# Optimization experiments

Hardware: AMD Instinct MI355X
Metric: run time of the kernel (lower is better)

Reference implementation:

```python
import jax, jax.numpy as jnp
import numpy as np

B, N, E, D, M, T, P, HS, HN, C, NH = 64, 1024, 512, 1024, 16, 12, 2048, 2048, 64, 4, 8
EPS = 1e-8


def _ln(x, g, b):
    m = x.mean(-1, keepdims=True)
    v = ((x - m) ** 2).mean(-1, keepdims=True)
    return (x - m) / jnp.sqrt(v + 1e-5) * g + b


def _glu(x):
    a, b = jnp.split(x, 2, axis=-1)
    return a * jax.nn.sigmoid(b)


def setup_inputs() -> dict:
    key = jax.random.key(0)
    ks = jax.random.split(key, 24)
    s = 0.02
    rn = lambda k, sh: jax.random.normal(k, sh, jnp.float32) * s
    inp = {
        'kv_tokens': jax.random.normal(ks[0], (B, N, E), jnp.float32),
        'raw_r_act': jnp.full((P,), -10.0, jnp.float32),  # no_decay_init
        'raw_r_out': jnp.full((P,), -10.0, jnp.float32),
        'q_w': rn(ks[1], (E, P)), 'q_b': jnp.zeros((E,), jnp.float32),
        'in_proj_w': rn(ks[2], (3 * E, E)), 'in_proj_b': jnp.zeros((3 * E,), jnp.float32),
        'out_proj_w': rn(ks[3], (E, E)), 'out_proj_b': jnp.zeros((E,), jnp.float32),
        'z_ln_g': jnp.ones((D,), jnp.float32), 'z_ln_b': jnp.zeros((D,), jnp.float32),
        'o_ln_g': jnp.ones((E,), jnp.float32), 'o_ln_b': jnp.zeros((E,), jnp.float32),
        'gate_w': rn(ks[4], (D, D + E)), 'gate_b': jnp.zeros((D,), jnp.float32),
        'cand_w': rn(ks[5], (D, D + E)), 'cand_b': jnp.zeros((D,), jnp.float32),
        'syn1_w': rn(ks[6], (HS, D + E)), 'syn1_b': jnp.zeros((HS,), jnp.float32),
        'syn2_w': rn(ks[7], (D, HS)), 'syn2_b': jnp.zeros((D,), jnp.float32),
        'nlm1_w': rn(ks[8], (D, M, 2 * HN)), 'nlm1_b': jnp.zeros((D, 2 * HN), jnp.float32),
        'nlm2_w': rn(ks[9], (D, HN, 2)), 'nlm2_b': jnp.zeros((D, 2), jnp.float32),
        'head_w': rn(ks[10], (C, P)), 'head_b': jnp.zeros((C,), jnp.float32),
        'act_left': jax.random.randint(ks[11], (P,), 0, D),
        'act_right': jax.random.randint(ks[12], (P,), 0, D),
        'out_left': jax.random.randint(ks[13], (P,), 0, D),
        'out_right': jax.random.randint(ks[14], (P,), 0, D),
    }
    return inp


def reference(kv_tokens, raw_r_act, raw_r_out, q_w, q_b, in_proj_w, in_proj_b,
              out_proj_w, out_proj_b, z_ln_g, z_ln_b, o_ln_g, o_ln_b,
              gate_w, gate_b, cand_w, cand_b, syn1_w, syn1_b, syn2_w, syn2_b,
              nlm1_w, nlm1_b, nlm2_w, nlm2_b, head_w, head_b,
              act_left, act_right, out_left, out_right):
    dh = E // NH
    scale = 1.0 / np.sqrt(dh).astype(np.float32)
    Wq, Wk, Wv = jnp.split(in_proj_w, 3, axis=0)
    bq, bk, bv = jnp.split(in_proj_b, 3, axis=0)
    # K/V are tick-invariant: project once.
    k = (kv_tokens @ Wk.T + bk).reshape(B, N, NH, dh).transpose(0, 2, 1, 3)  # [B,H,N,dh]
    v = (kv_tokens @ Wv.T + bv).reshape(B, N, NH, dh).transpose(0, 2, 1, 3)
    decay_a = jnp.exp(-jax.nn.softplus(raw_r_act))[None, :]
    decay_o = jnp.exp(-jax.nn.softplus(raw_r_out))[None, :]

    z0 = jnp.zeros((B, D), kv_tokens.dtype)
    A0 = jnp.zeros((B, D, M), kv_tokens.dtype)
    # init_state with z0 == 0 -> alpha 0, beta 1, synch 0
    a_a0 = z0[:, act_left] * z0[:, act_right]
    b_a0 = jnp.ones_like(a_a0)
    s_a0 = a_a0 / jnp.sqrt(b_a0 + EPS)
    a_o0 = z0[:, out_left] * z0[:, out_right]
    b_o0 = jnp.ones_like(a_o0)

    def tick(carry, _):
        z, A, a_a, b_a, s_a, a_o, b_o = carry
        # attention query from action sync
        q = s_a @ q_w.T + q_b                                  # [B,E]
        qh = (q @ Wq.T + bq).reshape(B, NH, 1, dh)
        scores = jnp.einsum('bhqd,bhnd->bhqn', qh, k) * scale  # [B,H,1,N]
        attn = jax.nn.softmax(scores, axis=-1)
        o = jnp.einsum('bhqn,bhnd->bhqd', attn, v).reshape(B, E)
        o = o @ out_proj_w.T + out_proj_b
        o = _ln(o, o_ln_g, o_ln_b)                             # LN on o
        zn = _ln(z, z_ln_g, z_ln_b)                            # LN on z
        # gated fusion
        u = jnp.concatenate([zn, o], axis=-1)
        g = jax.nn.sigmoid(u @ gate_w.T + gate_b)
        h = jnp.tanh(u @ cand_w.T + cand_b)
        z_bar = (1.0 - g) * zn + g * h
        fused = jnp.concatenate([z_bar, o], axis=-1)           # [B,D+E]
        # synapse MLP -> pre-activation
        pre = jax.nn.gelu(fused @ syn1_w.T + syn1_b, approximate=False) @ syn2_w.T + syn2_b
        A = jnp.concatenate([A[:, :, 1:], pre[:, :, None]], axis=-1)  # shift history
        # deep NLM (per-neuron SuperLinear + GLU, twice)
        h1 = _glu(jnp.einsum('bdm,dmh->bdh', A, nlm1_w) + nlm1_b)
        z = _glu(jnp.einsum('bdh,dho->bdo', h1, nlm2_w) + nlm2_b)[..., 0]
        # decayed pair synchronisation updates
        a_a = decay_a * a_a + z[:, act_left] * z[:, act_right]
        b_a = decay_a * b_a + 1.0
        s_a = a_a / jnp.sqrt(b_a + EPS)
        a_o = decay_o * a_o + z[:, out_left] * z[:, out_right]
        b_o = decay_o * b_o + 1.0
        s_o = a_o / jnp.sqrt(b_o + EPS)
        logits = s_o @ head_w.T + head_b                       # [B,C]
        return (z, A, a_a, b_a, s_a, a_o, b_o), (logits, z)

    carry0 = (z0, A0, a_a0, b_a0, s_a0, a_o0, b_o0)
    _, (logits_t, z_t) = jax.lax.scan(tick, carry0, None, length=T)
    logits_ticks = jnp.transpose(logits_t, (1, 2, 0))          # [B,C,T]
    p = jnp.clip(jax.nn.softmax(logits_ticks, axis=1), 1e-8, None)
    ent = -(p * jnp.log(p)).sum(axis=1)
    certainty = 1.0 - ent / np.float32(np.log(C))              # [B,T]
    z_ticks = jnp.transpose(z_t, (1, 0, 2))                    # [B,T,D]
    return logits_ticks, certainty, z_ticks
```

## Files before the change

### kernel.cpp

```cpp
#include <hip/hip_runtime.h>
#include <hip/hip_bf16.h>

#define B_ 64
#define N_ 1024
#define E_ 512
#define D_ 1024
#define M_ 16
#define T_ 12
#define P_ 2048
#define HS_ 2048
#define HN_ 64
#define C_ 4
#define NH_ 8
#define DH_ 64

typedef __attribute__((ext_vector_type(8))) short bf16x8;
typedef __attribute__((ext_vector_type(4))) float f32x4;

__device__ __forceinline__ float bf2f(unsigned int u) {
    union { unsigned int i; float f; } c; c.i = (u & 0xffffu) << 16; return c.f;
}
__device__ __forceinline__ unsigned short f2bf(float f) {
    union { float f; unsigned int i; } c; c.f = f;
    unsigned int x = c.i;
    unsigned int r = x + 0x7fffu + ((x >> 16) & 1u);
    return (unsigned short)(r >> 16);
}

__global__ void init_kernel(unsigned short* s_a_bf, float* a_a, float* b_a, float* a_o, float* b_o, float* z) {
    int i = blockIdx.x * 256 + threadIdx.x;
    if (i < B_ * P_) { a_a[i] = 0.f; b_a[i] = 1.f; a_o[i] = 0.f; b_o[i] = 1.f; s_a_bf[i] = 0; }
    if (i < B_ * D_) z[i] = 0.f;
}

__global__ __launch_bounds__(256) void cvt_bf16_kernel(const float* __restrict__ in,
                                                       unsigned short* __restrict__ out, int n4) {
    int i = blockIdx.x * 256 + threadIdx.x;
    if (i < n4) {
        float4 v = ((const float4*)in)[i];
        ushort4 o;
        o.x = f2bf(v.x); o.y = f2bf(v.y); o.z = f2bf(v.z); o.w = f2bf(v.w);
        ((ushort4*)out)[i] = o;
    }
}

__global__ __launch_bounds__(256) void cvt_ilv_kernel(const float* __restrict__ g,
                                                      const float* __restrict__ c,
                                                      unsigned short* __restrict__ out) {
    int r = blockIdx.x;
    const float* src = (r & 1) ? (c + (size_t)(r >> 1) * 1536) : (g + (size_t)(r >> 1) * 1536);
    for (int k = threadIdx.x * 4; k < 1536; k += 1024) {
        float4 v = *(const float4*)(src + k);
        ushort4 o;
        o.x = f2bf(v.x); o.y = f2bf(v.y); o.z = f2bf(v.z); o.w = f2bf(v.w);
        *(ushort4*)(out + (size_t)r * 1536 + k) = o;
    }
}

__global__ __launch_bounds__(256) void transpose_cvt_kernel(const float* __restrict__ in,
                                                            unsigned short* __restrict__ out,
                                                            int R, int Ccols) {
    __shared__ float tb[32][33];
    int c0 = blockIdx.x * 32, r0 = blockIdx.y * 32;
    int tx = threadIdx.x & 31, ty = threadIdx.x >> 5;
#pragma unroll
    for (int i = 0; i < 32; i += 8) tb[ty + i][tx] = in[(size_t)(r0 + ty + i) * Ccols + c0 + tx];
    __syncthreads();
#pragma unroll
    for (int i = 0; i < 32; i += 8) out[(size_t)(c0 + ty + i) * R + r0 + tx] = f2bf(tb[tx][ty + i]);
}

__global__ __launch_bounds__(256) void bcomb_kernel(const float* __restrict__ in_proj_w,
                                                    const float* __restrict__ in_proj_b,
                                                    const float* __restrict__ q_b,
                                                    float* __restrict__ bc) {
    int e = blockIdx.x * 256 + threadIdx.x;
    if (e < E_) {
        const float* wr = in_proj_w + (size_t)e * E_;
        float s = in_proj_b[e];
        for (int k = 0; k < E_; k += 4) {
            float4 w4 = *(const float4*)(wr + k);
            float4 q4 = *(const float4*)(q_b + k);
            s += w4.x * q4.x + w4.y * q4.y + w4.z * q4.z + w4.w * q4.w;
        }
        bc[e] = s;
    }
}

template <bool HAS_BIAS>
__global__ __launch_bounds__(256) void gemm_bt_kernel(const unsigned short* __restrict__ A,
                                                      const unsigned short* __restrict__ Bt,
                                                      const float* __restrict__ bias,
                                                      unsigned short* __restrict__ C,
                                                      int M, int N, int K) {
    __shared__ __align__(16) unsigned short ldsA[2][4096];
    __shared__ __align__(16) unsigned short ldsB[2][4096];
    int id = blockIdx.y * gridDim.x + blockIdx.x;
    int nwg = gridDim.x * gridDim.y;
    int swz = (id & 7) * (nwg >> 3) + (id >> 3);
    int bx = swz % gridDim.x, by = swz / gridDim.x;
    int m0 = by * 128;
    int n0 = bx * 128;
    int tid = threadIdx.x;
    int wv = tid >> 6, l = tid & 63;
    int wr = wv >> 1, wc = wv & 1;
    int lr = l & 15, lg = l >> 4;
    f32x4 acc[4][4] = {};

    auto stage = [&](int buf, int kt) {
        int k0 = kt * 32;
#pragma unroll
        for (int i = 0; i < 2; i++) {
            int tsk = tid + 256 * i;
            int r = tsk >> 2, g = tsk & 3;
            int gs = (g ^ (r & 3)) * 8;
            __builtin_amdgcn_global_load_lds(
                (const __attribute__((address_space(1))) void*)(A + (size_t)(m0 + r) * K + k0 + gs),
                (__attribute__((address_space(3))) void*)&ldsA[buf][tsk * 8], 16, 0, 0);
        }
#pragma unroll
        for (int i = 0; i < 2; i++) {
            int tsk = tid + 256 * i;
            int r = tsk >> 2, g = tsk & 3;
            int gs = (g ^ (r & 3)) * 8;
            __builtin_amdgcn_global_load_lds(
                (const __attribute__((address_space(1))) void*)(Bt + (size_t)(n0 + r) * K + k0 + gs),
                (__attribute__((address_space(3))) void*)&ldsB[buf][tsk * 8], 16, 0, 0);
        }
    };

    int nt = K >> 5;
    stage(0, 0);
    for (int t = 0; t < nt; t++) {
        int cur = t & 1;
        if (t + 1 < nt) {
            stage(cur ^ 1, t + 1);
            asm volatile("s_waitcnt vmcnt(4)" ::: "memory");
        } else {
            asm volatile("s_waitcnt vmcnt(0)" ::: "memory");
        }
        __builtin_amdgcn_s_barrier();
        bf16x8 af[4], bfr[4];
#pragma unroll
        for (int mi = 0; mi < 4; mi++) {
            int r = wr * 64 + mi * 16 + lr;
            af[mi] = *(const bf16x8*)&ldsA[cur][r * 32 + ((lg ^ (r & 3)) << 3)];
        }
#pragma unroll
        for (int ni = 0; ni < 4; ni++) {
            int c = wc * 64 + ni * 16 + lr;
            bfr[ni] = *(const bf16x8*)&ldsB[cur][c * 32 + ((lg ^ (c & 3)) << 3)];
        }
#pragma unroll
        for (int mi = 0; mi < 4; mi++)
#pragma unroll
            for (int ni = 0; ni < 4; ni++)
                acc[mi][ni] = __builtin_amdgcn_mfma_f32_16x16x32_bf16(af[mi], bfr[ni], acc[mi][ni], 0, 0, 0);
        __builtin_amdgcn_s_barrier();
    }
#pragma unroll
    for (int ni = 0; ni < 4; ni++) {
        int col = n0 + wc * 64 + ni * 16 + lr;
        float bv = HAS_BIAS ? bias[col] : 0.0f;
#pragma unroll
        for (int mi = 0; mi < 4; mi++) {
            int row = m0 + wr * 64 + mi * 16 + lg * 4;
#pragma unroll
            for (int r = 0; r < 4; r++) {
                C[(size_t)(row + r) * N + col] = f2bf(acc[mi][ni][r] + bv);
            }
        }
    }
}

template <int EPI>
__global__ __launch_bounds__(256) void gemmNK_kernel(const unsigned short* __restrict__ A,
                                                     const unsigned short* __restrict__ W,
                                                     const float* __restrict__ bias0,
                                                     const float* __restrict__ bias1,
                                                     const float* __restrict__ zn32,
                                                     void* __restrict__ outp,
                                                     int N, int K) {
    __shared__ __align__(16) unsigned short ldsA[4][2][2048];
    __shared__ __align__(16) unsigned short ldsB[4][2][512];
    int n0 = blockIdx.x * 16;
    int tid = threadIdx.x;
    int w = tid >> 6, l = tid & 63;
    int Kw = K >> 2;
    int kb = w * Kw;
    int lr = l & 15, lg = l >> 4;
    int ar = l >> 2, ag = l & 3;
    f32x4 acc[4] = {};

    auto stage = [&](int buf, int kt) {
        int k0 = kb + (kt << 5);
#pragma unroll
        for (int i = 0; i < 4; i++) {
            int row = i * 16 + ar;
            int gs = (ag ^ (row & 3)) << 3;
            __builtin_amdgcn_global_load_lds(
                (const __attribute__((address_space(1))) void*)(A + (size_t)row * K + k0 + gs),
                (__attribute__((address_space(3))) void*)&ldsA[w][buf][i * 512 + l * 8], 16, 0, 0);
        }
        {
            int col = ar;
            int gs = (ag ^ (col & 3)) << 3;
            __builtin_amdgcn_global_load_lds(
                (const __attribute__((address_space(1))) void*)(W + (size_t)(n0 + col) * K + k0 + gs),
                (__attribute__((address_space(3))) void*)&ldsB[w][buf][l * 8], 16, 0, 0);
        }
    };

    int nt = Kw >> 5;
    stage(0, 0);
    for (int t = 0; t < nt; t++) {
        int cur = t & 1;
        if (t + 1 < nt) {
            stage(cur ^ 1, t + 1);
            asm volatile("s_waitcnt vmcnt(5)" ::: "memory");
        } else {
            asm volatile("s_waitcnt vmcnt(0)" ::: "memory");
        }
        bf16x8 bf = *(const bf16x8*)&ldsB[w][cur][lr * 32 + ((lg ^ (lr & 3)) << 3)];
#pragma unroll
        for (int mi = 0; mi < 4; mi++) {
            int rr = mi * 16 + lr;
            bf16x8 af = *(const bf16x8*)&ldsA[w][cur][rr * 32 + ((lg ^ (rr & 3)) << 3)];
            acc[mi] = __builtin_amdgcn_mfma_f32_16x16x32_bf16(af, bf, acc[mi], 0, 0, 0);
        }
    }
    __syncthreads();
    float* red = (float*)&ldsA[0][0][0];
#pragma unroll
    for (int mi = 0; mi < 4; mi++) {
        int row = mi * 16 + lg * 4;
#pragma unroll
        for (int q = 0; q < 4; q++) red[w * 1024 + (row + q) * 16 + lr] = acc[mi][q];
    }
    __syncthreads();
    int b = tid >> 2, c4 = (tid & 3) << 2;
    f32x4 s = *(f32x4*)&red[b * 16 + c4];
#pragma unroll
    for (int ww = 1; ww < 4; ww++) {
        f32x4 v = *(f32x4*)&red[ww * 1024 + b * 16 + c4];
        s[0] += v[0]; s[1] += v[1]; s[2] += v[2]; s[3] += v[3];
    }
    int col = n0 + c4;
    if (EPI == 0) {
        unsigned short* out = (unsigned short*)outp;
        ushort4 o;
        o.x = f2bf(s[0] + bias0[col + 0]);
        o.y = f2bf(s[1] + bias0[col + 1]);
        o.z = f2bf(s[2] + bias0[col + 2]);
        o.w = f2bf(s[3] + bias0[col + 3]);
        *(ushort4*)(out + (size_t)b * N + col) = o;
    } else if (EPI == 1) {
        float* out = (float*)outp;
        *(f32x4*)(out + (size_t)b * N + col) = s;
    } else if (EPI == 2) {
        unsigned short* out = (unsigned short*)outp;
        int j0 = col >> 1;
#pragma unroll
        for (int pp = 0; pp < 2; pp++) {
            int j = j0 + pp;
            float g = 1.0f / (1.0f + expf(-(s[pp * 2] + bias0[j])));
            float h = tanhf(s[pp * 2 + 1] + bias1[j]);
            float zb = (1.0f - g) * zn32[(size_t)b * D_ + j] + g * h;
            out[(size_t)b * 1536 + j] = f2bf(zb);
        }
    } else if (EPI == 3) {
        unsigned short* out = (unsigned short*)outp;
        ushort4 o;
#pragma unroll
        for (int j = 0; j < 4; j++) {
            float pre = s[j] + bias0[col + j];
            float val = 0.5f * pre * (1.0f + erff(pre * 0.70710678118654752f));
            ((unsigned short*)&o)[j] = f2bf(val);
        }
        *(ushort4*)(out + (size_t)b * N + col) = o;
    } else {
        float* out = (float*)outp;
#pragma unroll
        for (int j = 0; j < 4; j++) {
            out[(size_t)(col + j) * 64 + b] = s[j] + bias0[col + j];
        }
    }
}

__device__ __forceinline__ float wave_max64(float v) {
#pragma unroll
    for (int off = 32; off >= 1; off >>= 1) v = fmaxf(v, __shfl_xor(v, off, 64));
    return v;
}
__device__ __forceinline__ float wave_sum64(float v) {
#pragma unroll
    for (int off = 32; off >= 1; off >>= 1) v += __shfl_xor(v, off, 64);
    return v;
}

__global__ __launch_bounds__(256) void attn_kernel(const unsigned short* __restrict__ kvbuf,
                                                   const unsigned short* __restrict__ qh_bf,
                                                   unsigned short* __restrict__ o_bf) {
    int bh = blockIdx.x;
    int b = bh >> 3, h = bh & 7;
    __shared__ float sc[N_];
    __shared__ float qv[DH_];
    __shared__ float red[8];
    __shared__ float opart[4][DH_];
    int tid = threadIdx.x;
    int w = tid >> 6, lane = tid & 63;
    if (tid < DH_) qv[tid] = bf2f(qh_bf[(size_t)b * E_ + h * DH_ + tid]);
    __syncthreads();
    const unsigned short* kb = kvbuf + (size_t)b * N_ * 1024 + h * DH_;
    float myv[4];
#pragma unroll
    for (int i = 0; i < 4; i++) {
        int n = tid + i * 256;
        const unsigned short* kr = kb + (size_t)n * 1024;
        float s = 0.f;
#pragma unroll
        for (int d = 0; d < DH_; d += 8) {
            uint4 pk = *(const uint4*)(kr + d);
            s += bf2f(pk.x) * qv[d + 0] + bf2f(pk.x >> 16) * qv[d + 1]
               + bf2f(pk.y) * qv[d + 2] + bf2f(pk.y >> 16) * qv[d + 3]
               + bf2f(pk.z) * qv[d + 4] + bf2f(pk.z >> 16) * qv[d + 5]
               + bf2f(pk.w) * qv[d + 6] + bf2f(pk.w >> 16) * qv[d + 7];
        }
        myv[i] = s * 0.125f;
    }
    float m = fmaxf(fmaxf(myv[0], myv[1]), fmaxf(myv[2], myv[3]));
    m = wave_max64(m);
    if (lane == 0) red[w] = m;
    __syncthreads();
    m = fmaxf(fmaxf(red[0], red[1]), fmaxf(red[2], red[3]));
    float s = 0.f;
#pragma unroll
    for (int i = 0; i < 4; i++) {
        float e = expf(myv[i] - m);
        sc[tid + i * 256] = e;
        s += e;
    }
    s = wave_sum64(s);
    if (lane == 0) red[4 + w] = s;
    __syncthreads();
    float inv = 1.0f / (red[4] + red[5] + red[6] + red[7]);
    const unsigned short* vb = kvbuf + (size_t)b * N_ * 1024 + E_ + h * DH_;
    int ng = lane >> 4, d4 = (lane & 15) << 2;
    float a0 = 0.f, a1 = 0.f, a2 = 0.f, a3 = 0.f;
    int n0 = w * 256;
    for (int i = 0; i < 64; i++) {
        int n = n0 + i * 4 + ng;
        uint2 pv = *(const uint2*)(vb + (size_t)n * 1024 + d4);
        float sv = sc[n];
        a0 += sv * bf2f(pv.x);
        a1 += sv * bf2f(pv.x >> 16);
        a2 += sv * bf2f(pv.y);
        a3 += sv * bf2f(pv.y >> 16);
    }
    a0 += __shfl_xor(a0, 16, 64); a0 += __shfl_xor(a0, 32, 64);
    a1 += __shfl_xor(a1, 16, 64); a1 += __shfl_xor(a1, 32, 64);
    a2 += __shfl_xor(a2, 16, 64); a2 += __shfl_xor(a2, 32, 64);
    a3 += __shfl_xor(a3, 16, 64); a3 += __shfl_xor(a3, 32, 64);
    if (lane < 16) {
        opart[w][d4 + 0] = a0;
        opart[w][d4 + 1] = a1;
        opart[w][d4 + 2] = a2;
        opart[w][d4 + 3] = a3;
    }
    __syncthreads();
    if (tid < DH_) {
        float r = (opart[0][tid] + opart[1][tid] + opart[2][tid] + opart[3][tid]) * inv;
        o_bf[(size_t)b * E_ + h * DH_ + tid] = f2bf(r);
    }
}

__global__ __launch_bounds__(256) void reduce_oln_kernel(const float* __restrict__ opre,
                                                         const float* __restrict__ bout,
                                                         const float* __restrict__ og,
                                                         const float* __restrict__ obv,
                                                         const float* __restrict__ z,
                                                         const float* __restrict__ zg,
                                                         const float* __restrict__ zbv,
                                                         unsigned short* __restrict__ u_bf,
                                                         unsigned short* __restrict__ fused_bf,
                                                         float* __restrict__ zn32) {
    int b = blockIdx.x, tid = threadIdx.x;
    __shared__ float red[16];
    float v[2];
#pragma unroll
    for (int i = 0; i < 2; i++) {
        int e = tid + i * 256;
        v[i] = opre[(size_t)b * E_ + e] + bout[e];
    }
    int w = tid >> 6, lane = tid & 63;
    float s1 = v[0] + v[1];
    float s2 = v[0] * v[0] + v[1] * v[1];
#pragma unroll
    for (int off = 32; off >= 1; off >>= 1) { s1 += __shfl_xor(s1, off, 64); s2 += __shfl_xor(s2, off, 64); }
    if (lane == 0) { red[w] = s1; red[4 + w] = s2; }
    __syncthreads();
    s1 = red[0] + red[1] + red[2] + red[3];
    s2 = red[4] + red[5] + red[6] + red[7];
    float mean = s1 * (1.0f / 512.0f);
    float var = s2 * (1.0f / 512.0f) - mean * mean;
    float rstd = 1.0f / sqrtf(var + 1e-5f);
#pragma unroll
    for (int i = 0; i < 2; i++) {
        int e = tid + i * 256;
        unsigned short val = f2bf((v[i] - mean) * rstd * og[e] + obv[e]);
        u_bf[(size_t)b * 1536 + D_ + e] = val;
        fused_bf[(size_t)b * 1536 + D_ + e] = val;
    }
    float zl[4];
    float t1 = 0.f, t2 = 0.f;
#pragma unroll
    for (int i = 0; i < 4; i++) {
        int d = tid + i * 256;
        zl[i] = z[(size_t)b * D_ + d];
        t1 += zl[i]; t2 += zl[i] * zl[i];
    }
#pragma unroll
    for (int off = 32; off >= 1; off >>= 1) { t1 += __shfl_xor(t1, off, 64); t2 += __shfl_xor(t2, off, 64); }
    __syncthreads();
    if (lane == 0) { red[8 + w] = t1; red[12 + w] = t2; }
    __syncthreads();
    t1 = red[8] + red[9] + red[10] + red[11];
    t2 = red[12] + red[13] + red[14] + red[15];
    float zmean = t1 * (1.0f / 1024.0f);
    float zvar = t2 * (1.0f / 1024.0f) - zmean * zmean;
    float zr = 1.0f / sqrtf(zvar + 1e-5f);
#pragma unroll
    for (int i = 0; i < 4; i++) {
        int d = tid + i * 256;
        float zn = (zl[i] - zmean) * zr * zg[d] + zbv[d];
        u_bf[(size_t)b * 1536 + d] = f2bf(zn);
        zn32[(size_t)b * D_ + d] = zn;
    }
}

template <int NT>
__global__ __launch_bounds__(256) void nlm_kernel(const float* __restrict__ AbufT,
                                                  const float* __restrict__ w1g,
                                                  const float* __restrict__ b1g,
                                                  const float* __restrict__ w2g,
                                                  const float* __restrict__ b2g,
                                                  float* __restrict__ z,
                                                  float* __restrict__ zt) {
    __shared__ float w1s[4][2048];
    __shared__ float b1s[4][128];
    __shared__ float w2s[4][128];
    __shared__ float b2s[4][2];
    int tid = threadIdx.x;
    int w = tid >> 6, lane = tid & 63;
    int d = blockIdx.x * 4 + w;
    for (int i = lane; i < 2048; i += 64) w1s[w][i] = w1g[(size_t)d * 2048 + i];
    for (int i = lane; i < 128; i += 64) {
        b1s[w][i] = b1g[(size_t)d * 128 + i];
        w2s[w][i] = w2g[(size_t)d * 128 + i];
    }
    if (lane < 2) b2s[w][lane] = b2g[d * 2 + lane];
    __syncthreads();
    const int b = lane;
    float av[NT];
#pragma unroll
    for (int s = 0; s < NT; s++) av[s] = AbufT[((size_t)s * D_ + d) * 64 + b];
    constexpr int moff = M_ - NT;
    float o0 = b2s[w][0], o1 = b2s[w][1];
    for (int hh = 0; hh < 64; hh++) {
        float a = b1s[w][hh], bb = b1s[w][hh + 64];
#pragma unroll
        for (int s = 0; s < NT; s++) {
            float x = av[s];
            a += x * w1s[w][(s + moff) * 128 + hh];
            bb += x * w1s[w][(s + moff) * 128 + hh + 64];
        }
        float z1 = a / (1.0f + expf(-bb));
        o0 += z1 * w2s[w][hh * 2];
        o1 += z1 * w2s[w][hh * 2 + 1];
    }
    float zv = o0 / (1.0f + expf(-o1));
    z[(size_t)b * D_ + d] = zv;
    zt[((size_t)b * T_ + (NT - 1)) * D_ + d] = zv;
}

__global__ __launch_bounds__(256) void synchead_kernel(const float* __restrict__ z,
                                                       const int* __restrict__ act_l, const int* __restrict__ act_r,
                                                       const int* __restrict__ out_l, const int* __restrict__ out_r,
                                                       const float* __restrict__ raw_a, const float* __restrict__ raw_o,
                                                       const float* __restrict__ head_w, const float* __restrict__ head_b,
                                                       float* __restrict__ a_a, float* __restrict__ b_a,
                                                       unsigned short* __restrict__ s_a_bf,
                                                       float* __restrict__ a_o, float* __restrict__ b_o,
                                                       float* __restrict__ out_logits, float* __restrict__ out_cert, int t) {
    int b = blockIdx.x, tid = threadIdx.x;
    __shared__ float zv[D_];
    __shared__ float red[4][4];
    for (int i = tid; i < D_; i += 256) zv[i] = z[(size_t)b * D_ + i];
    __syncthreads();
    float l0 = 0.f, l1 = 0.f, l2 = 0.f, l3 = 0.f;
    for (int p = tid; p < P_; p += 256) {
        size_t ip = (size_t)b * P_ + p;
        float zl = zv[act_l[p]], zr = zv[act_r[p]];
        float da = 1.0f / (1.0f + expf(raw_a[p]));
        float aa = da * a_a[ip] + zl * zr;
        float ba = da * b_a[ip] + 1.0f;
        a_a[ip] = aa; b_a[ip] = ba;
        s_a_bf[(size_t)b * P_ + p] = f2bf(aa / sqrtf(ba + 1e-8f));
        float zlo = zv[out_l[p]], zro = zv[out_r[p]];
        float dz = 1.0f / (1.0f + expf(raw_o[p]));
        float ao = dz * a_o[ip] + zlo * zro;
        float bo = dz * b_o[ip] + 1.0f;
        a_o[ip] = ao; b_o[ip] = bo;
        float so = ao / sqrtf(bo + 1e-8f);
        l0 += so * head_w[p];
        l1 += so * head_w[P_ + p];
        l2 += so * head_w[2 * P_ + p];
        l3 += so * head_w[3 * P_ + p];
    }
    int w = tid >> 6, lane = tid & 63;
#pragma unroll
    for (int off = 32; off >= 1; off >>= 1) {
        l0 += __shfl_xor(l0, off, 64);
        l1 += __shfl_xor(l1, off, 64);
        l2 += __shfl_xor(l2, off, 64);
        l3 += __shfl_xor(l3, off, 64);
    }
    if (lane == 0) { red[w][0] = l0; red[w][1] = l1; red[w][2] = l2; red[w][3] = l3; }
    __syncthreads();
    if (tid == 0) {
        float lg[4];
#pragma unroll
        for (int c = 0; c < 4; c++) {
            lg[c] = red[0][c] + red[1][c] + red[2][c] + red[3][c] + head_b[c];
            out_logits[((size_t)b * C_ + c) * T_ + t] = lg[c];
        }
        float m = fmaxf(fmaxf(lg[0], lg[1]), fmaxf(lg[2], lg[3]));
        float e0 = expf(lg[0] - m), e1 = expf(lg[1] - m), e2 = expf(lg[2] - m), e3 = expf(lg[3] - m);
        float inv = 1.0f / (e0 + e1 + e2 + e3);
        float ent = 0.f, pp;
        pp = fmaxf(e0 * inv, 1e-8f); ent -= pp * logf(pp);
        pp = fmaxf(e1 * inv, 1e-8f); ent -= pp * logf(pp);
        pp = fmaxf(e2 * inv, 1e-8f); ent -= pp * logf(pp);
        pp = fmaxf(e3 * inv, 1e-8f); ent -= pp * logf(pp);
        out_cert[(size_t)b * T_ + t] = 1.0f - ent * (1.0f / 1.3862943611198906f);
    }
}

extern "C" void kernel_launch(void* const* d_in, const int* in_sizes, int n_in,
                              void* d_out, int out_size, void* d_ws, size_t ws_size,
                              hipStream_t stream) {
    const float* kv_tokens  = (const float*)d_in[0];
    const float* raw_r_act  = (const float*)d_in[1];
    const float* raw_r_out  = (const float*)d_in[2];
    const float* q_w        = (const float*)d_in[3];
    const float* q_b        = (const float*)d_in[4];
    const float* in_proj_w  = (const float*)d_in[5];
    const float* in_proj_b  = (const float*)d_in[6];
    const float* out_proj_w = (const float*)d_in[7];
    const float* out_proj_b = (const float*)d_in[8];
    const float* z_ln_g     = (const float*)d_in[9];
    const float* z_ln_b     = (const float*)d_in[10];
    const float* o_ln_g     = (const float*)d_in[11];
    const float* o_ln_b     = (const float*)d_in[12];
    const float* gate_w     = (const float*)d_in[13];
    const float* gate_b     = (const float*)d_in[14];
    const float* cand_w     = (const float*)d_in[15];
    const float* cand_b     = (const float*)d_in[16];
    const float* syn1_w     = (const float*)d_in[17];
    const float* syn1_b     = (const float*)d_in[18];
    const float* syn2_w     = (const float*)d_in[19];
    const float* syn2_b     = (const float*)d_in[20];
    const float* nlm1_w     = (const float*)d_in[21];
    const float* nlm1_b     = (const float*)d_in[22];
    const float* nlm2_w     = (const float*)d_in[23];
    const float* nlm2_b     = (const float*)d_in[24];
    const float* head_w     = (const float*)d_in[25];
    const float* head_b     = (const float*)d_in[26];
    const int* act_l        = (const int*)d_in[27];
    const int* act_r        = (const int*)d_in[28];
    const int* out_l        = (const int*)d_in[29];
    const int* out_r        = (const int*)d_in[30];

    float* out = (float*)d_out;
    float* out_logits = out;
    float* out_cert = out + B_ * C_ * T_;
    float* out_zt = out_cert + B_ * T_;

    char* ws = (char*)d_ws;
    size_t off = 0;
    auto alloc = [&](size_t bytes) { void* p = ws + off; off += (bytes + 255) & ~(size_t)255; return p; };
    unsigned short* kvbuf   = (unsigned short*)alloc((size_t)B_ * N_ * 1024 * 2);
    unsigned short* kv_bf   = (unsigned short*)alloc((size_t)B_ * N_ * E_ * 2);
    unsigned short* Wkv_bf  = (unsigned short*)alloc((size_t)1024 * E_ * 2);
    unsigned short* Wq_bf   = (unsigned short*)alloc((size_t)E_ * E_ * 2);
    unsigned short* qwT_bf  = (unsigned short*)alloc((size_t)P_ * E_ * 2);
    unsigned short* Wc_bf   = (unsigned short*)alloc((size_t)E_ * P_ * 2);
    unsigned short* Wgc_bf  = (unsigned short*)alloc((size_t)2048 * 1536 * 2);
    unsigned short* Ws1_bf  = (unsigned short*)alloc((size_t)2048 * 1536 * 2);
    unsigned short* Ws2_bf  = (unsigned short*)alloc((size_t)1024 * 2048 * 2);
    unsigned short* Wout_bf = (unsigned short*)alloc((size_t)E_ * E_ * 2);
    float* b_comb = (float*)alloc(E_ * 4);
    unsigned short* s_a_bf  = (unsigned short*)alloc((size_t)B_ * P_ * 2);
    unsigned short* qh_bf   = (unsigned short*)alloc((size_t)B_ * E_ * 2);
    unsigned short* o_bf    = (unsigned short*)alloc((size_t)B_ * E_ * 2);
    unsigned short* u_bf    = (unsigned short*)alloc((size_t)B_ * 1536 * 2);
    unsigned short* fused_bf= (unsigned short*)alloc((size_t)B_ * 1536 * 2);
    unsigned short* tbuf_bf = (unsigned short*)alloc((size_t)B_ * HS_ * 2);
    float* opre = (float*)alloc((size_t)B_ * E_ * 4);
    float* zn32 = (float*)alloc((size_t)B_ * D_ * 4);
    float* a_a  = (float*)alloc((size_t)B_ * P_ * 4);
    float* b_a  = (float*)alloc((size_t)B_ * P_ * 4);
    float* a_o  = (float*)alloc((size_t)B_ * P_ * 4);
    float* b_o  = (float*)alloc((size_t)B_ * P_ * 4);
    float* zbuf = (float*)alloc((size_t)B_ * D_ * 4);
    float* AbufT = (float*)alloc((size_t)T_ * D_ * B_ * 4);

    init_kernel<<<512, 256, 0, stream>>>(s_a_bf, a_a, b_a, a_o, b_o, zbuf);

    cvt_bf16_kernel<<<(1024 * E_ / 4 + 255) / 256, 256, 0, stream>>>(in_proj_w + (size_t)E_ * E_, Wkv_bf, 1024 * E_ / 4);
    cvt_bf16_kernel<<<(E_ * E_ / 4 + 255) / 256, 256, 0, stream>>>(in_proj_w, Wq_bf, E_ * E_ / 4);
    cvt_ilv_kernel<<<2048, 256, 0, stream>>>(gate_w, cand_w, Wgc_bf);
    cvt_bf16_kernel<<<(2048 * 1536 / 4 + 255) / 256, 256, 0, stream>>>(syn1_w, Ws1_bf, 2048 * 1536 / 4);
    cvt_bf16_kernel<<<(1024 * 2048 / 4 + 255) / 256, 256, 0, stream>>>(syn2_w, Ws2_bf, 1024 * 2048 / 4);
    cvt_bf16_kernel<<<(E_ * E_ / 4 + 255) / 256, 256, 0, stream>>>(out_proj_w, Wout_bf, E_ * E_ / 4);
    transpose_cvt_kernel<<<dim3(P_ / 32, E_ / 32), 256, 0, stream>>>(q_w, qwT_bf, E_, P_);
    bcomb_kernel<<<2, 256, 0, stream>>>(in_proj_w, in_proj_b, q_b, b_comb);
    gemm_bt_kernel<false><<<dim3(P_ / 128, E_ / 128), 256, 0, stream>>>(Wq_bf, qwT_bf, nullptr, Wc_bf, E_, P_, E_);

    cvt_bf16_kernel<<<(B_ * N_ * E_ / 4) / 256, 256, 0, stream>>>(kv_tokens, kv_bf, B_ * N_ * E_ / 4);
    gemm_bt_kernel<true><<<dim3(8, 512), 256, 0, stream>>>(kv_bf, Wkv_bf, in_proj_b + E_,
                                                           kvbuf, B_ * N_, 1024, E_);

    for (int t = 0; t < T_; t++) {
        gemmNK_kernel<0><<<32, 256, 0, stream>>>(s_a_bf, Wc_bf, b_comb, nullptr, nullptr, qh_bf, E_, P_);
        attn_kernel<<<B_ * NH_, 256, 0, stream>>>(kvbuf, qh_bf, o_bf);
        gemmNK_kernel<1><<<32, 256, 0, stream>>>(o_bf, Wout_bf, nullptr, nullptr, nullptr, opre, E_, E_);
        reduce_oln_kernel<<<64, 256, 0, stream>>>(opre, out_proj_b, o_ln_g, o_ln_b,
                                                  zbuf, z_ln_g, z_ln_b, u_bf, fused_bf, zn32);
        gemmNK_kernel<2><<<128, 256, 0, stream>>>(u_bf, Wgc_bf, gate_b, cand_b, zn32, fused_bf, 2048, 1536);
        gemmNK_kernel<3><<<128, 256, 0, stream>>>(fused_bf, Ws1_bf, syn1_b, nullptr, nullptr, tbuf_bf, 2048, 1536);
        gemmNK_kernel<4><<<64, 256, 0, stream>>>(tbuf_bf, Ws2_bf, syn2_b, nullptr, nullptr,
                                                 AbufT + (size_t)t * D_ * 64, 1024, 2048);
        switch (t) {
            case 0:  nlm_kernel<1><<<256, 256, 0, stream>>>(AbufT, nlm1_w, nlm1_b, nlm2_w, nlm2_b, zbuf, out_zt); break;
            case 1:  nlm_kernel<2><<<256, 256, 0, stream>>>(AbufT, nlm1_w, nlm1_b, nlm2_w, nlm2_b, zbuf, out_zt); break;
            case 2:  nlm_kernel<3><<<256, 256, 0, stream>>>(AbufT, nlm1_w, nlm1_b, nlm2_w, nlm2_b, zbuf, out_zt); break;
            case 3:  nlm_kernel<4><<<256, 256, 0, stream>>>(AbufT, nlm1_w, nlm1_b, nlm2_w, nlm2_b, zbuf, out_zt); break;
            case 4:  nlm_kernel<5><<<256, 256, 0, stream>>>(AbufT, nlm1_w, nlm1_b, nlm2_w, nlm2_b, zbuf, out_zt); break;
            case 5:  nlm_kernel<6><<<256, 256, 0, stream>>>(AbufT, nlm1_w, nlm1_b, nlm2_w, nlm2_b, zbuf, out_zt); break;
            case 6:  nlm_kernel<7><<<256, 256, 0, stream>>>(AbufT, nlm1_w, nlm1_b, nlm2_w, nlm2_b, zbuf, out_zt); break;
            case 7:  nlm_kernel<8><<<256, 256, 0, stream>>>(AbufT, nlm1_w, nlm1_b, nlm2_w, nlm2_b, zbuf, out_zt); break;
            case 8:  nlm_kernel<9><<<256, 256, 0, stream>>>(AbufT, nlm1_w, nlm1_b, nlm2_w, nlm2_b, zbuf, out_zt); break;
            case 9:  nlm_kernel<10><<<256, 256, 0, stream>>>(AbufT, nlm1_w, nlm1_b, nlm2_w, nlm2_b, zbuf, out_zt); break;
            case 10: nlm_kernel<11><<<256, 256, 0, stream>>>(AbufT, nlm1_w, nlm1_b, nlm2_w, nlm2_b, zbuf, out_zt); break;
            default: nlm_kernel<12><<<256, 256, 0, stream>>>(AbufT, nlm1_w, nlm1_b, nlm2_w, nlm2_b, zbuf, out_zt); break;
        }
        synchead_kernel<<<64, 256, 0, stream>>>(zbuf, act_l, act_r, out_l, out_r, raw_r_act, raw_r_out,
                                                head_w, head_b, a_a, b_a, s_a_bf, a_o, b_o,
                                                out_logits, out_cert, t);
    }
}
```

Measured before the change: 1.438 ms.

## Fold key projection into per-head query map to skip computing K

Stops materializing the key projection of all tokens. Instead it precomputes per-head products of Wk^T with the combined query weight (Gmat) and a bias term. Each tick then maps s_a to a per-head 512-wide query in token space and scores raw tokens directly with MFMA. Only V is projected up front, which halves the large B*N projection GEMM and the kvbuf traffic. The trade-off is a larger per-tick query GEMM (4096 wide) and an MFMA scoring pass that reads the full 512-dim tokens each tick instead of 64-dim keys. The nlm1 weights are also converted to bf16 to cut per-tick weight loads.

```diff
diff --git a/kernel.cpp b/kernel.cpp
--- a/kernel.cpp
+++ b/kernel.cpp
@@ -85,6 +85,19 @@
         }
         bc[e] = s;
     }
+}
+
+__global__ __launch_bounds__(256) void br_kernel(const float* __restrict__ in_proj_w,
+                                                 const float* __restrict__ bc,
+                                                 float* __restrict__ br) {
+    int g = blockIdx.x * 256 + threadIdx.x;
+    int h = g >> 9, j = g & 511;
+    const float* Wk = in_proj_w + (size_t)E_ * E_;
+    float s = 0.f;
+    for (int e = 0; e < 64; e++) {
+        s += Wk[(size_t)(h * 64 + e) * E_ + j] * bc[h * 64 + e];
+    }
+    br[g] = s;
 }
 
 template <bool HAS_BIAS>
@@ -173,6 +186,87 @@
     }
 }
 
+__global__ __launch_bounds__(256) void gemm_hb_kernel(const unsigned short* __restrict__ A0, int lda, size_t sAz,
+                                                      const unsigned short* __restrict__ B0, int ldb, size_t sBz,
+                                                      unsigned short* __restrict__ C0, int ldc, size_t sCz,
+                                                      int K) {
+    __shared__ __align__(16) unsigned short ldsA[2][4096];
+    __shared__ __align__(16) unsigned short ldsB[2][4096];
+    const unsigned short* A = A0 + blockIdx.z * sAz;
+    const unsigned short* Bt = B0 + blockIdx.z * sBz;
+    unsigned short* C = C0 + blockIdx.z * sCz;
+    int m0 = blockIdx.y * 128, n0 = blockIdx.x * 128;
+    int tid = threadIdx.x;
+    int wv = tid >> 6, l = tid & 63;
+    int wr = wv >> 1, wc = wv & 1;
+    int lr = l & 15, lg = l >> 4;
+    f32x4 acc[4][4] = {};
+
+    auto stage = [&](int buf, int kt) {
+        int k0 = kt * 32;
+#pragma unroll
+        for (int i = 0; i < 2; i++) {
+            int tsk = tid + 256 * i;
+            int r = tsk >> 2, g = tsk & 3;
+            int gs = (g ^ (r & 3)) * 8;
+            __builtin_amdgcn_global_load_lds(
+                (const __attribute__((address_space(1))) void*)(A + (size_t)(m0 + r) * lda + k0 + gs),
+                (__attribute__((address_space(3))) void*)&ldsA[buf][tsk * 8], 16, 0, 0);
+        }
+#pragma unroll
+        for (int i = 0; i < 2; i++) {
+            int tsk = tid + 256 * i;
+            int r = tsk >> 2, g = tsk & 3;
+            int gs = (g ^ (r & 3)) * 8;
+            __builtin_amdgcn_global_load_lds(
+                (const __attribute__((address_space(1))) void*)(Bt + (size_t)(n0 + r) * ldb + k0 + gs),
+                (__attribute__((address_space(3))) void*)&ldsB[buf][tsk * 8], 16, 0, 0);
+        }
+    };
+
+    int nt = K >> 5;
+    stage(0, 0);
+    for (int t = 0; t < nt; t++) {
+        int cur = t & 1;
+        if (t + 1 < nt) {
+            stage(cur ^ 1, t + 1);
+            asm volatile("s_waitcnt vmcnt(4)" ::: "memory");
+        } else {
+            asm volatile("s_waitcnt vmcnt(0)" ::: "memory");
+        }
+        __builtin_amdgcn_s_barrier();
+        bf16x8 af[4], bfr[4];
+#pragma unroll
+        for (int mi = 0; mi < 4; mi++) {
+            int r = wr * 64 + mi * 16 + lr;
+            af[mi] = *(const bf16x8*)&ldsA[cur][r * 32 + ((lg ^ (r & 3)) << 3)];
+        }
+#pragma unroll
+        for (int ni = 0; ni < 4; ni++) {
+            int c = wc * 64 + ni * 16 + lr;
+            bfr[ni] = *(const bf16x8*)&ldsB[cur][c * 32 + ((lg ^ (c & 3)) << 3)];
+        }
+#pragma unroll
+        for (int mi = 0; mi < 4; mi++)
+#pragma unroll
+            for (int ni = 0; ni < 4; ni++)
+                acc[mi][ni] = __builtin_amdgcn_mfma_f32_16x16x32_bf16(af[mi], bfr[ni], acc[mi][ni], 0, 0, 0);
+        __builtin_amdgcn_s_barrier();
+    }
+#pragma unroll
+    for (int ni = 0; ni < 4; ni++) {
+        int col = n0 + wc * 64 + ni * 16 + lr;
+#pragma unroll
+        for (int mi = 0; mi < 4; mi++) {
+            int row = m0 + wr * 64 + mi * 16 + lg * 4;
+#pragma unroll
+            for (int r = 0; r < 4; r++) {
+                C[(size_t)(row + r) * ldc + col] = f2bf(acc[mi][ni][r]);
+            }
+        }
+    }
+}
+
 template <int EPI>
 __global__ __launch_bounds__(256) void gemmNK_kernel(const unsigned short* __restrict__ A,
                                                      const unsigned short* __restrict__ W,
@@ -249,10 +343,10 @@
     if (EPI == 0) {
         unsigned short* out = (unsigned short*)outp;
         ushort4 o;
-        o.x = f2bf(s[0] + bias0[col + 0]);
-        o.y = f2bf(s[1] + bias0[col + 1]);
-        o.z = f2bf(s[2] + bias0[col + 2]);
-        o.w = f2bf(s[3] + bias0[col + 3]);
+        o.x = f2bf(0.125f * (s[0] + bias0[col + 0]));
+        o.y = f2bf(0.125f * (s[1] + bias0[col + 1]));
+        o.z = f2bf(0.125f * (s[2] + bias0[col + 2]));
+        o.w = f2bf(0.125f * (s[3] + bias0[col + 3]));
         *(ushort4*)(out + (size_t)b * N + col) = o;
     } else if (EPI == 1) {
         float* out = (float*)outp;
@@ -287,49 +381,57 @@
     }
 }
 
-__device__ __forceinline__ float wave_max64(float v) {
-#pragma unroll
-    for (int off = 32; off >= 1; off >>= 1) v = fmaxf(v, __shfl_xor(v, off, 64));
-    return v;
-}
-__device__ __forceinline__ float wave_sum64(float v) {
-#pragma unroll
-    for (int off = 32; off >= 1; off >>= 1) v += __shfl_xor(v, off, 64);
-    return v;
-}
-
-__global__ __launch_bounds__(256) void attn_kernel(const unsigned short* __restrict__ kvbuf,
-                                                   const unsigned short* __restrict__ qh_bf,
-                                                   unsigned short* __restrict__ o_bf) {
+__global__ __launch_bounds__(256) void scoreX_kernel(const unsigned short* __restrict__ X,
+                                                     const unsigned short* __restrict__ r_bf,
+                                                     float* __restrict__ S) {
+    int b = blockIdx.y;
+    int n0 = blockIdx.x * 128;
+    int tid = threadIdx.x;
+    int wv = tid >> 6, l = tid & 63;
+    int lr = l & 15, lg = l >> 4;
+    const unsigned short* Xb = X + ((size_t)b * 1024 + n0) * 512;
+    const unsigned short* rb = r_bf + (size_t)b * 4096 + (size_t)(lr & 7) * 512 + lg * 8;
+    f32x4 acc[2] = {};
+#pragma unroll
+    for (int kt = 0; kt < 16; kt++) {
+        int k0 = kt * 32;
+        bf16x8 bfrag = *(const bf16x8*)(rb + k0);
+#pragma unroll
+        for (int mi = 0; mi < 2; mi++) {
+            int row = (wv * 2 + mi) * 16 + lr;
+            bf16x8 afrag = *(const bf16x8*)(Xb + (size_t)row * 512 + k0 + lg * 8);
+            acc[mi] = __builtin_amdgcn_mfma_f32_16x16x32_bf16(afrag, bfrag, acc[mi], 0, 0, 0);
+        }
+    }
+    if (lr < 8) {
+#pragma unroll
+        for (int mi = 0; mi < 2; mi++) {
+            int rowbase = (wv * 2 + mi) * 16 + lg * 4;
+#pragma unroll
+            for (int q = 0; q < 4; q++) {
+                S[((size_t)b * 8 + lr) * 1024 + n0 + rowbase + q] = acc[mi][q];
+            }
+        }
+    }
+}
+
+__global__ __launch_bounds__(256) void attnV_kernel(const float* __restrict__ S,
+                                                    const unsigned short* __restrict__ vbuf,
+                                                    unsigned short* __restrict__ o_bf) {
     int bh = blockIdx.x;
     int b = bh >> 3, h = bh & 7;
     __shared__ float sc[N_];
-    __shared__ float qv[DH_];
     __shared__ float red[8];
     __shared__ float opart[4][DH_];
     int tid = threadIdx.x;
     int w = tid >> 6, lane = tid & 63;
-    if (tid < DH_) qv[tid] = bf2f(qh_bf[(size_t)b * E_ + h * DH_ + tid]);
-    __syncthreads();
-    const unsigned short* kb = kvbuf + (size_t)b * N_ * 1024 + h * DH_;
+    const float* Ss = S + ((size_t)b * 8 + h) * 1024;
     float myv[4];
 #pragma unroll
-    for (int i = 0; i < 4; i++) {
-        int n = tid + i * 256;
-        const unsigned short* kr = kb + (size_t)n * 1024;
-        float s = 0.f;
-#pragma unroll
-        for (int d = 0; d < DH_; d += 8) {
-            uint4 pk = *(const uint4*)(kr + d);
-            s += bf2f(pk.x) * qv[d + 0] + bf2f(pk.x >> 16) * qv[d + 1]
-               + bf2f(pk.y) * qv[d + 2] + bf2f(pk.y >> 16) * qv[d + 3]
-               + bf2f(pk.z) * qv[d + 4] + bf2f(pk.z >> 16) * qv[d + 5]
-               + bf2f(pk.w) * qv[d + 6] + bf2f(pk.w >> 16) * qv[d + 7];
-        }
-        myv[i] = s * 0.125f;
-    }
+    for (int i = 0; i < 4; i++) myv[i] = Ss[tid + i * 256];
     float m = fmaxf(fmaxf(myv[0], myv[1]), fmaxf(myv[2], myv[3]));
-    m = wave_max64(m);
+#pragma unroll
+    for (int off = 32; off >= 1; off >>= 1) m = fmaxf(m, __shfl_xor(m, off, 64));
     if (lane == 0) red[w] = m;
     __syncthreads();
     m = fmaxf(fmaxf(red[0], red[1]), fmaxf(red[2], red[3]));
@@ -340,17 +442,18 @@
         sc[tid + i * 256] = e;
         s += e;
     }
-    s = wave_sum64(s);
+#pragma unroll
+    for (int off = 32; off >= 1; off >>= 1) s += __shfl_xor(s, off, 64);
     if (lane == 0) red[4 + w] = s;
     __syncthreads();
     float inv = 1.0f / (red[4] + red[5] + red[6] + red[7]);
-    const unsigned short* vb = kvbuf + (size_t)b * N_ * 1024 + E_ + h * DH_;
+    const unsigned short* vb = vbuf + (size_t)b * 1024 * 512 + h * DH_;
     int ng = lane >> 4, d4 = (lane & 15) << 2;
     float a0 = 0.f, a1 = 0.f, a2 = 0.f, a3 = 0.f;
     int n0 = w * 256;
     for (int i = 0; i < 64; i++) {
         int n = n0 + i * 4 + ng;
-        uint2 pv = *(const uint2*)(vb + (size_t)n * 1024 + d4);
+        uint2 pv = *(const uint2*)(vb + (size_t)n * 512 + d4);
         float sv = sc[n];
         a0 += sv * bf2f(pv.x);
         a1 += sv * bf2f(pv.x >> 16);
@@ -440,7 +543,7 @@
 
 template <int NT>
 __global__ __launch_bounds__(256) void nlm_kernel(const float* __restrict__ AbufT,
-                                                  const float* __restrict__ w1g,
+                                                  const unsigned short* __restrict__ w1g_bf,
                                                   const float* __restrict__ b1g,
                                                   const float* __restrict__ w2g,
                                                   const float* __restrict__ b2g,
@@ -453,7 +556,11 @@
     int tid = threadIdx.x;
     int w = tid >> 6, lane = tid & 63;
     int d = blockIdx.x * 4 + w;
-    for (int i = lane; i < 2048; i += 64) w1s[w][i] = w1g[(size_t)d * 2048 + i];
+    for (int i = lane * 2; i < 2048; i += 128) {
+        unsigned int pk = *(const unsigned int*)(w1g_bf + (size_t)d * 2048 + i);
+        w1s[w][i] = bf2f(pk);
+        w1s[w][i + 1] = bf2f(pk >> 16);
+    }
     for (int i = lane; i < 128; i += 64) {
         b1s[w][i] = b1g[(size_t)d * 128 + i];
         w2s[w][i] = w2g[(size_t)d * 128 + i];
@@ -589,19 +696,24 @@
     char* ws = (char*)d_ws;
     size_t off = 0;
     auto alloc = [&](size_t bytes) { void* p = ws + off; off += (bytes + 255) & ~(size_t)255; return p; };
-    unsigned short* kvbuf   = (unsigned short*)alloc((size_t)B_ * N_ * 1024 * 2);
     unsigned short* kv_bf   = (unsigned short*)alloc((size_t)B_ * N_ * E_ * 2);
-    unsigned short* Wkv_bf  = (unsigned short*)alloc((size_t)1024 * E_ * 2);
+    unsigned short* vbuf    = (unsigned short*)alloc((size_t)B_ * N_ * E_ * 2);
+    unsigned short* Wv_bf   = (unsigned short*)alloc((size_t)E_ * E_ * 2);
     unsigned short* Wq_bf   = (unsigned short*)alloc((size_t)E_ * E_ * 2);
+    unsigned short* WkT_bf  = (unsigned short*)alloc((size_t)E_ * E_ * 2);
     unsigned short* qwT_bf  = (unsigned short*)alloc((size_t)P_ * E_ * 2);
-    unsigned short* Wc_bf   = (unsigned short*)alloc((size_t)E_ * P_ * 2);
+    unsigned short* WcT_bf  = (unsigned short*)alloc((size_t)P_ * E_ * 2);
+    unsigned short* Gmat    = (unsigned short*)alloc((size_t)4096 * P_ * 2);
     unsigned short* Wgc_bf  = (unsigned short*)alloc((size_t)2048 * 1536 * 2);
     unsigned short* Ws1_bf  = (unsigned short*)alloc((size_t)2048 * 1536 * 2);
     unsigned short* Ws2_bf  = (unsigned short*)alloc((size_t)1024 * 2048 * 2);
     unsigned short* Wout_bf = (unsigned short*)alloc((size_t)E_ * E_ * 2);
-    float* b_comb = (float*)alloc(E_ * 4);
+    unsigned short* nlm1w_bf= (unsigned short*)alloc((size_t)1024 * 2048 * 2);
+    float* bc   = (float*)alloc(E_ * 4);
+    float* brv  = (float*)alloc(4096 * 4);
     unsigned short* s_a_bf  = (unsigned short*)alloc((size_t)B_ * P_ * 2);
-    unsigned short* qh_bf   = (unsigned short*)alloc((size_t)B_ * E_ * 2);
+    unsigned short* r_bf    = (unsigned short*)alloc((size_t)B_ * 4096 * 2);
+    float* Sbuf = (float*)alloc((size_t)B_ * 8 * N_ * 4);
     unsigned short* o_bf    = (unsigned short*)alloc((size_t)B_ * E_ * 2);
     unsigned short* u_bf    = (unsigned short*)alloc((size_t)B_ * 1536 * 2);
     unsigned short* fused_bf= (unsigned short*)alloc((size_t)B_ * 1536 * 2);
@@ -617,23 +729,29 @@
 
     init_kernel<<<512, 256, 0, stream>>>(s_a_bf, a_a, b_a, a_o, b_o, zbuf);
 
-    cvt_bf16_kernel<<<(1024 * E_ / 4 + 255) / 256, 256, 0, stream>>>(in_proj_w + (size_t)E_ * E_, Wkv_bf, 1024 * E_ / 4);
-    cvt_bf16_kernel<<<(E_ * E_ / 4 + 255) / 256, 256, 0, stream>>>(in_proj_w, Wq_bf, E_ * E_ / 4);
+    cvt_bf16_kernel<<<(B_ * N_ * E_ / 4) / 256, 256, 0, stream>>>(kv_tokens, kv_bf, B_ * N_ * E_ / 4);
+    cvt_bf16_kernel<<<256, 256, 0, stream>>>(in_proj_w + (size_t)2 * E_ * E_, Wv_bf, E_ * E_ / 4);
+    cvt_bf16_kernel<<<256, 256, 0, stream>>>(in_proj_w, Wq_bf, E_ * E_ / 4);
+    transpose_cvt_kernel<<<dim3(16, 16), 256, 0, stream>>>(in_proj_w + (size_t)E_ * E_, WkT_bf, E_, E_);
+    transpose_cvt_kernel<<<dim3(P_ / 32, E_ / 32), 256, 0, stream>>>(q_w, qwT_bf, E_, P_);
+    bcomb_kernel<<<2, 256, 0, stream>>>(in_proj_w, in_proj_b, q_b, bc);
+    br_kernel<<<16, 256, 0, stream>>>(in_proj_w, bc, brv);
+    gemm_bt_kernel<false><<<dim3(E_ / 128, P_ / 128), 256, 0, stream>>>(qwT_bf, Wq_bf, nullptr, WcT_bf, P_, E_, E_);
+    gemm_hb_kernel<<<dim3(P_ / 128, E_ / 128, NH_), 256, 0, stream>>>(WkT_bf, E_, 64,
+                                                                      WcT_bf, E_, 64,
+                                                                      Gmat, P_, (size_t)512 * P_, 64);
     cvt_ilv_kernel<<<2048, 256, 0, stream>>>(gate_w, cand_w, Wgc_bf);
     cvt_bf16_kernel<<<(2048 * 1536 / 4 + 255) / 256, 256, 0, stream>>>(syn1_w, Ws1_bf, 2048 * 1536 / 4);
     cvt_bf16_kernel<<<(1024 * 2048 / 4 + 255) / 256, 256, 0, stream>>>(syn2_w, Ws2_bf, 1024 * 2048 / 4);
-    cvt_bf16_kernel<<<(E_ * E_ / 4 + 255) / 256, 256, 0, stream>>>(out_proj_w, Wout_bf, E_ * E_ / 4);
-    transpose_cvt_kernel<<<dim3(P_ / 32, E_ / 32), 256, 0, stream>>>(q_w, qwT_bf, E_, P_);
-    bcomb_kernel<<<2, 256, 0, stream>>>(in_proj_w, in_proj_b, q_b, b_comb);
-    gemm_bt_kernel<false><<<dim3(P_ / 128, E_ / 128), 256, 0, stream>>>(Wq_bf, qwT_bf, nullptr, Wc_bf, E_, P_, E_);
-
-    cvt_bf16_kernel<<<(B_ * N_ * E_ / 4) / 256, 256, 0, stream>>>(kv_tokens, kv_bf, B_ * N_ * E_ / 4);
-    gemm_bt_kernel<true><<<dim3(8, 512), 256, 0, stream>>>(kv_bf, Wkv_bf, in_proj_b + E_,
-                                                           kvbuf, B_ * N_, 1024, E_);
+    cvt_bf16_kernel<<<(1024 * 2048 / 4 + 255) / 256, 256, 0, stream>>>(nlm1_w, nlm1w_bf, 1024 * 2048 / 4);
+    cvt_bf16_kernel<<<256, 256, 0, stream>>>(out_proj_w, Wout_bf, E_ * E_ / 4);
+    gemm_bt_kernel<true><<<dim3(E_ / 128, B_ * N_ / 128), 256, 0, stream>>>(kv_bf, Wv_bf, in_proj_b + 2 * E_,
+                                                                            vbuf, B_ * N_, E_, E_);
 
     for (int t = 0; t < T_; t++) {
-        gemmNK_kernel<0><<<32, 256, 0, stream>>>(s_a_bf, Wc_bf, b_comb, nullptr, nullptr, qh_bf, E_, P_);
-        attn_kernel<<<B_ * NH_, 256, 0, stream>>>(kvbuf, qh_bf, o_bf);
+        gemmNK_kernel<0><<<256, 256, 0, stream>>>(s_a_bf, Gmat, brv, nullptr, nullptr, r_bf, 4096, P_);
+        scoreX_kernel<<<dim3(8, 64), 256, 0, stream>>>(kv_bf, r_bf, Sbuf);
+        attnV_kernel<<<B_ * NH_, 256, 0, stream>>>(Sbuf, vbuf, o_bf);
         gemmNK_kernel<1><<<32, 256, 0, stream>>>(o_bf, Wout_bf, nullptr, nullptr, nullptr, opre, E_, E_);
         reduce_oln_kernel<<<64, 256, 0, stream>>>(opre, out_proj_b, o_ln_g, o_ln_b,
                                                   zbuf, z_ln_g, z_ln_b, u_bf, fused_bf, zn32);
@@ -642,18 +760,18 @@
         gemmNK_kernel<4><<<64, 256, 0, stream>>>(tbuf_bf, Ws2_bf, syn2_b, nullptr, nullptr,
                                                  AbufT + (size_t)t * D_ * 64, 1024, 2048);
         switch (t) {
-            case 0:  nlm_kernel<1><<<256, 256, 0, stream>>>(AbufT, nlm1_w, nlm1_b, nlm2_w, nlm2_b, zbuf, out_zt); break;
-            case 1:  nlm_kernel<2><<<256, 256, 0, stream>>>(AbufT, nlm1_w, nlm1_b, nlm2_w, nlm2_b, zbuf, out_zt); break;
-            case 2:  nlm_kernel<3><<<256, 256, 0, stream>>>(AbufT, nlm1_w, nlm1_b, nlm2_w, nlm2_b, zbuf, out_zt); break;
-            case 3:  nlm_kernel<4><<<256, 256, 0, stream>>>(AbufT, nlm1_w, nlm1_b, nlm2_w, nlm2_b, zbuf, out_zt); break;
-            case 4:  nlm_kernel<5><<<256, 256, 0, stream>>>(AbufT, nlm1_w, nlm1_b, nlm2_w, nlm2_b, zbuf, out_zt); break;
-            case 5:  nlm_kernel<6><<<256, 256, 0, stream>>>(AbufT, nlm1_w, nlm1_b, nlm2_w, nlm2_b, zbuf, out_zt); break;
-            case 6:  nlm_kernel<7><<<256, 256, 0, stream>>>(AbufT, nlm1_w, nlm1_b, nlm2_w, nlm2_b, zbuf, out_zt); break;
-            case 7:  nlm_kernel<8><<<256, 256, 0, stream>>>(AbufT, nlm1_w, nlm1_b, nlm2_w, nlm2_b, zbuf, out_zt); break;
-            case 8:  nlm_kernel<9><<<256, 256, 0, stream>>>(AbufT, nlm1_w, nlm1_b, nlm2_w, nlm2_b, zbuf, out_zt); break;
-            case 9:  nlm_kernel<10><<<256, 256, 0, stream>>>(AbufT, nlm1_w, nlm1_b, nlm2_w, nlm2_b, zbuf, out_zt); break;
-            case 10: nlm_kernel<11><<<256, 256, 0, stream>>>(AbufT, nlm1_w, nlm1_b, nlm2_w, nlm2_b, zbuf, out_zt); break;
-            default: nlm_kernel<12><<<256, 256, 0, stream>>>(AbufT, nlm1_w, nlm1_b, nlm2_w, nlm2_b, zbuf, out_zt); break;
+            case 0:  nlm_kernel<1><<<256, 256, 0, stream>>>(AbufT, nlm1w_bf, nlm1_b, nlm2_w, nlm2_b, zbuf, out_zt); break;
+            case 1:  nlm_kernel<2><<<256, 256, 0, stream>>>(AbufT, nlm1w_bf, nlm1_b, nlm2_w, nlm2_b, zbuf, out_zt); break;
+            case 2:  nlm_kernel<3><<<256, 256, 0, stream>>>(AbufT, nlm1w_bf, nlm1_b, nlm2_w, nlm2_b, zbuf, out_zt); break;
+            case 3:  nlm_kernel<4><<<256, 256, 0, stream>>>(AbufT, nlm1w_bf, nlm1_b, nlm2_w, nlm2_b, zbuf, out_zt); break;
+            case 4:  nlm_kernel<5><<<256, 256, 0, stream>>>(AbufT, nlm1w_bf, nlm1_b, nlm2_w, nlm2_b, zbuf, out_zt); break;
+            case 5:  nlm_kernel<6><<<256, 256, 0, stream>>>(AbufT, nlm1w_bf, nlm1_b, nlm2_w, nlm2_b, zbuf, out_zt); break;
+            case 6:  nlm_kernel<7><<<256, 256, 0, stream>>>(AbufT, nlm1w_bf, nlm1_b, nlm2_w, nlm2_b, zbuf, out_zt); break;
+            case 7:  nlm_kernel<8><<<256, 256, 0, stream>>>(AbufT, nlm1w_bf, nlm1_b, nlm2_w, nlm2_b, zbuf, out_zt); break;
+            case 8:  nlm_kernel<9><<<256, 256, 0, stream>>>(AbufT, nlm1w_bf, nlm1_b, nlm2_w, nlm2_b, zbuf, out_zt); break;
+            case 9:  nlm_kernel<10><<<256, 256, 0, stream>>>(AbufT, nlm1w_bf, nlm1_b, nlm2_w, nlm2_b, zbuf, out_zt); break;
+            case 10: nlm_kernel<11><<<256, 256, 0, stream>>>(AbufT, nlm1w_bf, nlm1_b, nlm2_w, nlm2_b, zbuf, out_zt); break;
+            default: nlm_kernel<12><<<256, 256, 0, stream>>>(AbufT, nlm1w_bf, nlm1_b, nlm2_w, nlm2_b, zbuf, out_zt); break;
         }
         synchead_kernel<<<64, 256, 0, stream>>>(zbuf, act_l, act_r, out_l, out_r, raw_r_act, raw_r_out,
                                                 head_w, head_b, a_a, b_a, s_a_bf, a_o, b_o,
```

Measured after the change: 1.340 ms. -6.8%, faster.
